# Kernel tuning notes

Measured on AMD Instinct MI355X. Metric: run time of the kernel, lower is better.

The kernel has to match this reference:

```python
import jax, jax.numpy as jnp
import numpy as np

HID = 128
IN = 4

def _lstm_cell(x, h, c, Wih, Whh, bih, bhh):
    # PyTorch LSTMCell: gates ordered i, f, g, o
    gates = x @ Wih.T + bih + h @ Whh.T + bhh  # [B, 4*HID]
    i, f, g, o = jnp.split(gates, 4, axis=-1)
    c_new = jax.nn.sigmoid(f) * c + jax.nn.sigmoid(i) * jnp.tanh(g)
    h_new = jax.nn.sigmoid(o) * jnp.tanh(c_new)
    return h_new, c_new


def setup_inputs() -> dict:
    key = jax.random.key(0)
    ks = jax.random.split(key, 12)
    T, B = 2048, 2048
    s = 1.0 / np.sqrt(HID)  # torch LSTMCell/Linear init scale (1/sqrt(hidden))
    u = lambda k, shape, sc: jax.random.uniform(k, shape, jnp.float32, -sc, sc)
    inp = {
        "input": jax.random.normal(ks[0], (T, B, IN), jnp.float32),
        "future": 0,
        "W_ih1": u(ks[1], (4 * HID, IN), s),
        "W_hh1": u(ks[2], (4 * HID, HID), s),
        "b_ih1": u(ks[3], (4 * HID,), s),
        "b_hh1": u(ks[4], (4 * HID,), s),
        "W_ih2": u(ks[5], (4 * HID, HID), s),
        "W_hh2": u(ks[6], (4 * HID, HID), s),
        "b_ih2": u(ks[7], (4 * HID,), s),
        "b_hh2": u(ks[8], (4 * HID,), s),
        "W_lin": u(ks[9], (IN, HID), s),
        "b_lin": u(ks[10], (IN,), s),
        "h0": jnp.zeros((B, HID), jnp.float32),
        "c0": jnp.zeros((B, HID), jnp.float32),
        "h02": jnp.zeros((B, HID), jnp.float32),
        "c02": jnp.zeros((B, HID), jnp.float32),
    }
    return inp


def reference(input, future, W_ih1, W_hh1, b_ih1, b_hh1, W_ih2, W_hh2, b_ih2, b_hh2,
              W_lin, b_lin, h0, c0, h02, c02):
    # alpha=1 default => teacher forcing on every step (branch never taken), future=0
    def step(carry, x_t):
        h1, c1, h2, c2 = carry
        h1, c1 = _lstm_cell(x_t, h1, c1, W_ih1, W_hh1, b_ih1, b_hh1)
        h2, c2 = _lstm_cell(h1, h2, c2, W_ih2, W_hh2, b_ih2, b_hh2)
        out = h2 @ W_lin.T + b_lin  # [B, 4]
        return (h1, c1, h2, c2), out

    _, outputs = jax.lax.scan(step, (h0, c0, h02, c02), input)
    return outputs  # [T, B, 4]
```

## Files before the change

kernel.cpp:

```cpp
#include <hip/hip_runtime.h>

#define T_STEPS 2048
#define BATCH   2048
#define HIDN    128

typedef short v8s __attribute__((ext_vector_type(8)));
typedef float v4f __attribute__((ext_vector_type(4)));
typedef unsigned short u16;
typedef unsigned int   u32;

#define LDS_W1    0
#define LDS_H1    131072
#define LDS_H2    (131072 + 8192)
#define LDS_TOTAL (131072 + 16384)

__device__ __forceinline__ u16 f2bf(float x) {
    u32 u = __float_as_uint(x);
    u32 r = (u + 0x7FFFu + ((u >> 16) & 1u)) >> 16;
    return (u16)r;
}
__device__ __forceinline__ float rcpf(float x) { return __builtin_amdgcn_rcpf(x); }
__device__ __forceinline__ float sigf(float x) { return rcpf(1.0f + __expf(-x)); }
__device__ __forceinline__ float tanhf_(float x) {
    float e = __expf(2.0f * x);
    return 1.0f - 2.0f * rcpf(e + 1.0f);
}
__device__ __forceinline__ int fragoff(int r, int k) {
    return ((k >> 5) << 10) + ((((k >> 3) & 3) * 16 + r) << 4) + ((k & 7) << 1);
}

__global__ __launch_bounds__(512, 2) void lstm_seq_kernel(
    const float* __restrict__ input,
    const float* __restrict__ W_ih1, const float* __restrict__ W_hh1,
    const float* __restrict__ b_ih1, const float* __restrict__ b_hh1,
    const float* __restrict__ W_ih2, const float* __restrict__ W_hh2,
    const float* __restrict__ b_ih2, const float* __restrict__ b_hh2,
    const float* __restrict__ W_lin, const float* __restrict__ b_lin,
    const float* __restrict__ h0,  const float* __restrict__ c0,
    const float* __restrict__ h02, const float* __restrict__ c02,
    float* __restrict__ out)
{
    extern __shared__ char smem[];
    const int tid = threadIdx.x;
    const int w   = tid >> 6;
    const int l   = tid & 63;
    const int u   = l & 15;
    const int q   = l >> 4;
    const int b0  = blockIdx.x * 8;
    const bool low = (q < 2);
    const int j   = w * 16 + u;

    for (int e = tid; e < 4096; e += 512)
        ((float*)(smem + LDS_H1))[e] = 0.0f;
    __syncthreads();
    for (int e = tid; e < 1024; e += 512) {
        int m = e >> 7, jj = e & 127;
        u16 hv1 = f2bf(h0 [(b0 + m) * HIDN + jj]);
        u16 hv2 = f2bf(h02[(b0 + m) * HIDN + jj]);
        int fo = fragoff(m, jj);
        *(u16*)(smem + LDS_H1 + 4096 + fo)       = hv1;
        *(u16*)(smem + LDS_H1 + 4096 + fo + 128) = hv1;
        *(u16*)(smem + LDS_H2 + 4096 + fo)       = hv2;
    }

    #pragma unroll
    for (int tl = 0; tl < 4; ++tl) {
        int r = tl * 128 + j;
        #pragma unroll
        for (int kt = 0; kt < 4; ++kt) {
            const float* src = W_hh1 + r * HIDN + kt * 32 + q * 8;
            v8s f;
            #pragma unroll
            for (int b = 0; b < 8; ++b) f[b] = (short)f2bf(src[b]);
            *(v8s*)(smem + LDS_W1 + (((w * 4 + tl) * 4 + kt) << 10) + l * 16) = f;
        }
    }

    v8s w2[4][8];
    #pragma unroll
    for (int tl = 0; tl < 4; ++tl) {
        int r = tl * 128 + j;
        #pragma unroll
        for (int kt = 0; kt < 8; ++kt) {
            const float* src = (kt < 4) ? (W_ih2 + r * HIDN + kt * 32 + q * 8)
                                        : (W_hh2 + r * HIDN + (kt - 4) * 32 + q * 8);
            v8s f;
            #pragma unroll
            for (int b = 0; b < 8; ++b) f[b] = (short)f2bf(src[b]);
            w2[tl][kt] = f;
        }
    }
    v8s wx[4];
    #pragma unroll
    for (int tl = 0; tl < 4; ++tl) {
        int r = tl * 128 + j;
        v8s f;
        #pragma unroll
        for (int b = 0; b < 8; ++b) {
            int k = q * 8 + b;
            f[b] = (k < 4) ? (short)f2bf(W_ih1[r * 4 + k]) : (short)0;
        }
        wx[tl] = f;
    }
    v8s wlin[4];
    if (w == 7) {
        #pragma unroll
        for (int kt = 0; kt < 4; ++kt) {
            v8s f;
            #pragma unroll
            for (int b = 0; b < 8; ++b) {
                int kk = kt * 32 + q * 8 + b;
                f[b] = (u < 4) ? (short)f2bf(W_lin[u * HIDN + kk]) : (short)0;
            }
            wlin[kt] = f;
        }
    }

    float bg[4];
    #pragma unroll
    for (int g = 0; g < 4; ++g)
        bg[g] = low ? (b_ih2[g * 128 + j] + b_hh2[g * 128 + j])
                    : (b_ih1[g * 128 + j] + b_hh1[g * 128 + j]);
    float blin = (w == 7 && u < 4) ? b_lin[u] : 0.0f;
    float c[4];
    #pragma unroll
    for (int d = 0; d < 4; ++d) {
        int m = low ? (4 * q + d) : (4 * (q - 2) + d);
        c[d] = low ? c02[(b0 + m) * HIDN + j] : c0[(b0 + m) * HIDN + j];
    }
    float4 xcur = {0, 0, 0, 0}, xnext = {0, 0, 0, 0};
    if (q == 0 && u >= 8)
        xcur = *(const float4*)(input + (long)(b0 + u - 8) * 4);

    const int cb = fragoff(0, j);
    __syncthreads();

    for (int s = 0; s <= T_STEPS; ++s) {
        const char* h1r = smem + LDS_H1 + ((s - 1) & 1) * 4096;
        const char* h2r = smem + LDS_H2 + (s & 1) * 4096;

        v8s a1[4];
        #pragma unroll
        for (int kt = 0; kt < 4; ++kt)
            a1[kt] = *(const v8s*)(h1r + (kt << 10) + l * 16);

        v4f accL2[4], accL1[4];

        if (s >= 1) {
            v8s a2[4];
            #pragma unroll
            for (int kt = 0; kt < 4; ++kt)
                a2[kt] = *(const v8s*)(h2r + (kt << 10) + l * 16);
            #pragma unroll
            for (int tl = 0; tl < 4; ++tl) {
                v4f a = {0.f, 0.f, 0.f, 0.f};
                #pragma unroll
                for (int kt = 0; kt < 4; ++kt)
                    a = __builtin_amdgcn_mfma_f32_16x16x32_bf16(a1[kt], w2[tl][kt], a, 0, 0, 0);
                #pragma unroll
                for (int kt = 0; kt < 4; ++kt)
                    a = __builtin_amdgcn_mfma_f32_16x16x32_bf16(a2[kt], w2[tl][kt + 4], a, 0, 0, 0);
                accL2[tl] = a;
            }
            if (w == 7 && s >= 2) {
                v4f oa = {0.f, 0.f, 0.f, 0.f};
                #pragma unroll
                for (int kt = 0; kt < 4; ++kt)
                    oa = __builtin_amdgcn_mfma_f32_16x16x32_bf16(a2[kt], wlin[kt], oa, 0, 0, 0);
                if (low && u < 4) {
                    #pragma unroll
                    for (int d = 0; d < 4; ++d)
                        out[((long)(s - 2) * BATCH + b0 + 4 * q + d) * 4 + u] = oa[d] + blin;
                }
            }
        }

        if (s < T_STEPS) {
            v8s ax = {0, 0, 0, 0, 0, 0, 0, 0};
            if (q == 0 && u >= 8) {
                ax[0] = (short)f2bf(xcur.x); ax[1] = (short)f2bf(xcur.y);
                ax[2] = (short)f2bf(xcur.z); ax[3] = (short)f2bf(xcur.w);
            }
            if (q == 0 && u >= 8 && s + 1 < T_STEPS)
                xnext = *(const float4*)(input + ((long)(s + 1) * BATCH + b0 + u - 8) * 4);
            #pragma unroll
            for (int tl = 0; tl < 4; ++tl) {
                v4f a = {0.f, 0.f, 0.f, 0.f};
                #pragma unroll
                for (int kt = 0; kt < 4; ++kt) {
                    v8s wf = *(const v8s*)(smem + LDS_W1 + (((w * 4 + tl) * 4 + kt) << 10) + l * 16);
                    a = __builtin_amdgcn_mfma_f32_16x16x32_bf16(a1[kt], wf, a, 0, 0, 0);
                }
                a = __builtin_amdgcn_mfma_f32_16x16x32_bf16(ax, wx[tl], a, 0, 0, 0);
                accL1[tl] = a;
            }
        }

        bool act_en = low ? (s >= 1) : (s < T_STEPS);
        if (act_en) {
            int rbase = low ? (4 * q) : (4 * (q - 2));
            char* hw = (char*)smem + (low ? (LDS_H2 + ((s - 1) & 1) * 4096)
                                          : (LDS_H1 + (s & 1) * 4096));
            #pragma unroll
            for (int d = 0; d < 4; ++d) {
                float gI = (low ? accL2[0][d] : accL1[0][d]) + bg[0];
                float gF = (low ? accL2[1][d] : accL1[1][d]) + bg[1];
                float gG = (low ? accL2[2][d] : accL1[2][d]) + bg[2];
                float gO = (low ? accL2[3][d] : accL1[3][d]) + bg[3];
                float si = sigf(gI), sf = sigf(gF), tg = tanhf_(gG), so = sigf(gO);
                c[d] = sf * c[d] + si * tg;
                float h = so * tanhf_(c[d]);
                u16 hb = f2bf(h);
                int r = rbase + d;
                *(u16*)(hw + cb + (r << 4)) = hb;
                if (!low) *(u16*)(hw + cb + (r << 4) + 128) = hb;
            }
        }
        xcur = xnext;
        __syncthreads();
    }

    if (w == 7) {
        const char* h2r = smem + LDS_H2 + ((T_STEPS - 1) & 1) * 4096;
        v4f oa = {0.f, 0.f, 0.f, 0.f};
        #pragma unroll
        for (int kt = 0; kt < 4; ++kt) {
            v8s a = *(const v8s*)(h2r + (kt << 10) + l * 16);
            oa = __builtin_amdgcn_mfma_f32_16x16x32_bf16(a, wlin[kt], oa, 0, 0, 0);
        }
        if (low && u < 4) {
            #pragma unroll
            for (int d = 0; d < 4; ++d)
                out[((long)(T_STEPS - 1) * BATCH + b0 + 4 * q + d) * 4 + u] = oa[d] + blin;
        }
    }
}

extern "C" void kernel_launch(void* const* d_in, const int* in_sizes, int n_in,
                              void* d_out, int out_size, void* d_ws, size_t ws_size,
                              hipStream_t stream) {
    const float* input = (const float*)d_in[0];
    const float* W_ih1 = (const float*)d_in[2];
    const float* W_hh1 = (const float*)d_in[3];
    const float* b_ih1 = (const float*)d_in[4];
    const float* b_hh1 = (const float*)d_in[5];
    const float* W_ih2 = (const float*)d_in[6];
    const float* W_hh2 = (const float*)d_in[7];
    const float* b_ih2 = (const float*)d_in[8];
    const float* b_hh2 = (const float*)d_in[9];
    const float* W_lin = (const float*)d_in[10];
    const float* b_lin = (const float*)d_in[11];
    const float* h0    = (const float*)d_in[12];
    const float* c0    = (const float*)d_in[13];
    const float* h02   = (const float*)d_in[14];
    const float* c02   = (const float*)d_in[15];
    float* out = (float*)d_out;

    (void)hipFuncSetAttribute((const void*)lstm_seq_kernel,
                              hipFuncAttributeMaxDynamicSharedMemorySize, LDS_TOTAL);
    lstm_seq_kernel<<<BATCH / 8, 512, LDS_TOTAL, stream>>>(
        input, W_ih1, W_hh1, b_ih1, b_hh1, W_ih2, W_hh2, b_ih2, b_hh2,
        W_lin, b_lin, h0, c0, h02, c02, out);
}
```

Before: 3.563 ms.

## Move most W_hh1 fragments into registers and interleave layer MFMAs

Three of the four k-tiles of W_hh1 now stay in registers, and only the last k-tile, the input weights and W_lin are kept in LDS. This cuts the LDS footprint and the number of LDS weight reads per step. The MFMA loop is restructured to walk k-tiles once and feed both layer-1 and layer-2 accumulators from each h1 fragment, so independent MFMA chains are interleaved. The activation code is split per layer. The cost is much higher VGPR pressure, which risks spilling or breaking the 2-blocks-per-CU launch bound.

```diff
diff --git a/kernel.cpp b/kernel.cpp
--- a/kernel.cpp
+++ b/kernel.cpp
@@ -9,10 +9,12 @@
 typedef unsigned short u16;
 typedef unsigned int   u32;
 
-#define LDS_W1    0
-#define LDS_H1    131072
-#define LDS_H2    (131072 + 8192)
-#define LDS_TOTAL (131072 + 16384)
+#define LDS_W1K3  0
+#define LDS_WX    32768
+#define LDS_WLIN  65536
+#define LDS_H1    69632
+#define LDS_H2    77824
+#define LDS_TOTAL 86016
 
 __device__ __forceinline__ u16 f2bf(float x) {
     u32 u = __float_as_uint(x);
@@ -66,13 +68,33 @@
     #pragma unroll
     for (int tl = 0; tl < 4; ++tl) {
         int r = tl * 128 + j;
+        {
+            const float* src = W_hh1 + r * HIDN + 3 * 32 + q * 8;
+            v8s f;
+            #pragma unroll
+            for (int b = 0; b < 8; ++b) f[b] = (short)f2bf(src[b]);
+            *(v8s*)(smem + LDS_W1K3 + ((w * 4 + tl) << 10) + l * 16) = f;
+        }
+        {
+            v8s f;
+            #pragma unroll
+            for (int b = 0; b < 8; ++b) {
+                int k = q * 8 + b;
+                f[b] = (k < 4) ? (short)f2bf(W_ih1[r * 4 + k]) : (short)0;
+            }
+            *(v8s*)(smem + LDS_WX + ((w * 4 + tl) << 10) + l * 16) = f;
+        }
+    }
+    if (w == 7) {
         #pragma unroll
         for (int kt = 0; kt < 4; ++kt) {
-            const float* src = W_hh1 + r * HIDN + kt * 32 + q * 8;
-            v8s f;
-            #pragma unroll
-            for (int b = 0; b < 8; ++b) f[b] = (short)f2bf(src[b]);
-            *(v8s*)(smem + LDS_W1 + (((w * 4 + tl) * 4 + kt) << 10) + l * 16) = f;
+            v8s f;
+            #pragma unroll
+            for (int b = 0; b < 8; ++b) {
+                int kk = kt * 32 + q * 8 + b;
+                f[b] = (u < 4) ? (short)f2bf(W_lin[u * HIDN + kk]) : (short)0;
+            }
+            *(v8s*)(smem + LDS_WLIN + (kt << 10) + l * 16) = f;
         }
     }
 
@@ -90,29 +112,17 @@
             w2[tl][kt] = f;
         }
     }
-    v8s wx[4];
+    v8s w1r[4][3];
     #pragma unroll
     for (int tl = 0; tl < 4; ++tl) {
         int r = tl * 128 + j;
-        v8s f;
-        #pragma unroll
-        for (int b = 0; b < 8; ++b) {
-            int k = q * 8 + b;
-            f[b] = (k < 4) ? (short)f2bf(W_ih1[r * 4 + k]) : (short)0;
-        }
-        wx[tl] = f;
-    }
-    v8s wlin[4];
-    if (w == 7) {
-        #pragma unroll
-        for (int kt = 0; kt < 4; ++kt) {
-            v8s f;
-            #pragma unroll
-            for (int b = 0; b < 8; ++b) {
-                int kk = kt * 32 + q * 8 + b;
-                f[b] = (u < 4) ? (short)f2bf(W_lin[u * HIDN + kk]) : (short)0;
-            }
-            wlin[kt] = f;
+        #pragma unroll
+        for (int kt = 0; kt < 3; ++kt) {
+            const float* src = W_hh1 + r * HIDN + kt * 32 + q * 8;
+            v8s f;
+            #pragma unroll
+            for (int b = 0; b < 8; ++b) f[b] = (short)f2bf(src[b]);
+            w1r[tl][kt] = f;
         }
     }
 
@@ -132,90 +142,109 @@
     if (q == 0 && u >= 8)
         xcur = *(const float4*)(input + (long)(b0 + u - 8) * 4);
 
-    const int cb = fragoff(0, j);
     __syncthreads();
 
     for (int s = 0; s <= T_STEPS; ++s) {
         const char* h1r = smem + LDS_H1 + ((s - 1) & 1) * 4096;
         const char* h2r = smem + LDS_H2 + (s & 1) * 4096;
-
-        v8s a1[4];
-        #pragma unroll
-        for (int kt = 0; kt < 4; ++kt)
-            a1[kt] = *(const v8s*)(h1r + (kt << 10) + l * 16);
-
-        v4f accL2[4], accL1[4];
-
-        if (s >= 1) {
-            v8s a2[4];
-            #pragma unroll
-            for (int kt = 0; kt < 4; ++kt)
-                a2[kt] = *(const v8s*)(h2r + (kt << 10) + l * 16);
-            #pragma unroll
-            for (int tl = 0; tl < 4; ++tl) {
-                v4f a = {0.f, 0.f, 0.f, 0.f};
+        const bool doL1 = (s < T_STEPS);
+        const bool doL2 = (s >= 1);
+
+        if (q == 0 && u >= 8 && s + 1 < T_STEPS)
+            xnext = *(const float4*)(input + ((long)(s + 1) * BATCH + b0 + u - 8) * 4);
+
+        v4f acc1[4] = {{0,0,0,0},{0,0,0,0},{0,0,0,0},{0,0,0,0}};
+        v4f acc2[4] = {{0,0,0,0},{0,0,0,0},{0,0,0,0},{0,0,0,0}};
+
+        #pragma unroll
+        for (int kt = 0; kt < 4; ++kt) {
+            v8s a1k = *(const v8s*)(h1r + (kt << 10) + l * 16);
+            if (doL2) {
                 #pragma unroll
-                for (int kt = 0; kt < 4; ++kt)
-                    a = __builtin_amdgcn_mfma_f32_16x16x32_bf16(a1[kt], w2[tl][kt], a, 0, 0, 0);
+                for (int tl = 0; tl < 4; ++tl)
+                    acc2[tl] = __builtin_amdgcn_mfma_f32_16x16x32_bf16(a1k, w2[tl][kt], acc2[tl], 0, 0, 0);
+            }
+            if (doL1) {
+                if (kt < 3) {
+                    #pragma unroll
+                    for (int tl = 0; tl < 4; ++tl)
+                        acc1[tl] = __builtin_amdgcn_mfma_f32_16x16x32_bf16(a1k, w1r[tl][kt], acc1[tl], 0, 0, 0);
+                } else {
+                    #pragma unroll
+                    for (int tl = 0; tl < 4; ++tl) {
+                        v8s wf = *(const v8s*)(smem + LDS_W1K3 + ((w * 4 + tl) << 10) + l * 16);
+                        acc1[tl] = __builtin_amdgcn_mfma_f32_16x16x32_bf16(a1k, wf, acc1[tl], 0, 0, 0);
+                    }
+                }
+            }
+        }
+
+        v4f oa = {0.f, 0.f, 0.f, 0.f};
+        if (doL2) {
+            #pragma unroll
+            for (int kt = 0; kt < 4; ++kt) {
+                v8s a2k = *(const v8s*)(h2r + (kt << 10) + l * 16);
                 #pragma unroll
-                for (int kt = 0; kt < 4; ++kt)
-                    a = __builtin_amdgcn_mfma_f32_16x16x32_bf16(a2[kt], w2[tl][kt + 4], a, 0, 0, 0);
-                accL2[tl] = a;
-            }
-            if (w == 7 && s >= 2) {
-                v4f oa = {0.f, 0.f, 0.f, 0.f};
+                for (int tl = 0; tl < 4; ++tl)
+                    acc2[tl] = __builtin_amdgcn_mfma_f32_16x16x32_bf16(a2k, w2[tl][kt + 4], acc2[tl], 0, 0, 0);
+                if (w == 7) {
+                    v8s wl = *(const v8s*)(smem + LDS_WLIN + (kt << 10) + l * 16);
+                    oa = __builtin_amdgcn_mfma_f32_16x16x32_bf16(a2k, wl, oa, 0, 0, 0);
+                }
+            }
+            if (w == 7 && s >= 2 && low && u < 4) {
                 #pragma unroll
-                for (int kt = 0; kt < 4; ++kt)
-                    oa = __builtin_amdgcn_mfma_f32_16x16x32_bf16(a2[kt], wlin[kt], oa, 0, 0, 0);
-                if (low && u < 4) {
-                    #pragma unroll
-                    for (int d = 0; d < 4; ++d)
-                        out[((long)(s - 2) * BATCH + b0 + 4 * q + d) * 4 + u] = oa[d] + blin;
-                }
-            }
-        }
-
-        if (s < T_STEPS) {
+                for (int d = 0; d < 4; ++d)
+                    out[((long)(s - 2) * BATCH + b0 + 4 * q + d) * 4 + u] = oa[d] + blin;
+            }
+        }
+
+        if (low && doL2) {
+            char* hw = (char*)smem + LDS_H2 + ((s - 1) & 1) * 4096;
+            #pragma unroll
+            for (int d = 0; d < 4; ++d) {
+                float gI = acc2[0][d] + bg[0];
+                float gF = acc2[1][d] + bg[1];
+                float gG = acc2[2][d] + bg[2];
+                float gO = acc2[3][d] + bg[3];
+                float si = sigf(gI), sf = sigf(gF), tg = tanhf_(gG), so = sigf(gO);
+                c[d] = sf * c[d] + si * tg;
+                u16 hb = f2bf(so * tanhf_(c[d]));
+                int r = 4 * q + d;
+                *(u16*)(hw + fragoff(r, j)) = hb;
+            }
+        }
+
+        if (doL1) {
             v8s ax = {0, 0, 0, 0, 0, 0, 0, 0};
             if (q == 0 && u >= 8) {
                 ax[0] = (short)f2bf(xcur.x); ax[1] = (short)f2bf(xcur.y);
                 ax[2] = (short)f2bf(xcur.z); ax[3] = (short)f2bf(xcur.w);
             }
-            if (q == 0 && u >= 8 && s + 1 < T_STEPS)
-                xnext = *(const float4*)(input + ((long)(s + 1) * BATCH + b0 + u - 8) * 4);
             #pragma unroll
             for (int tl = 0; tl < 4; ++tl) {
-                v4f a = {0.f, 0.f, 0.f, 0.f};
-                #pragma unroll
-                for (int kt = 0; kt < 4; ++kt) {
-                    v8s wf = *(const v8s*)(smem + LDS_W1 + (((w * 4 + tl) * 4 + kt) << 10) + l * 16);
-                    a = __builtin_amdgcn_mfma_f32_16x16x32_bf16(a1[kt], wf, a, 0, 0, 0);
-                }
-                a = __builtin_amdgcn_mfma_f32_16x16x32_bf16(ax, wx[tl], a, 0, 0, 0);
-                accL1[tl] = a;
-            }
-        }
-
-        bool act_en = low ? (s >= 1) : (s < T_STEPS);
-        if (act_en) {
-            int rbase = low ? (4 * q) : (4 * (q - 2));
-            char* hw = (char*)smem + (low ? (LDS_H2 + ((s - 1) & 1) * 4096)
-                                          : (LDS_H1 + (s & 1) * 4096));
+                v8s wxf = *(const v8s*)(smem + LDS_WX + ((w * 4 + tl) << 10) + l * 16);
+                acc1[tl] = __builtin_amdgcn_mfma_f32_16x16x32_bf16(ax, wxf, acc1[tl], 0, 0, 0);
+            }
+        }
+
+        if (!low && doL1) {
+            char* hw = (char*)smem + LDS_H1 + (s & 1) * 4096;
             #pragma unroll
             for (int d = 0; d < 4; ++d) {
-                float gI = (low ? accL2[0][d] : accL1[0][d]) + bg[0];
-                float gF = (low ? accL2[1][d] : accL1[1][d]) + bg[1];
-                float gG = (low ? accL2[2][d] : accL1[2][d]) + bg[2];
-                float gO = (low ? accL2[3][d] : accL1[3][d]) + bg[3];
+                float gI = acc1[0][d] + bg[0];
+                float gF = acc1[1][d] + bg[1];
+                float gG = acc1[2][d] + bg[2];
+                float gO = acc1[3][d] + bg[3];
                 float si = sigf(gI), sf = sigf(gF), tg = tanhf_(gG), so = sigf(gO);
                 c[d] = sf * c[d] + si * tg;
-                float h = so * tanhf_(c[d]);
-                u16 hb = f2bf(h);
-                int r = rbase + d;
-                *(u16*)(hw + cb + (r << 4)) = hb;
-                if (!low) *(u16*)(hw + cb + (r << 4) + 128) = hb;
-            }
-        }
+                u16 hb = f2bf(so * tanhf_(c[d]));
+                int r = 4 * (q - 2) + d;
+                *(u16*)(hw + fragoff(r, j))     = hb;
+                *(u16*)(hw + fragoff(r + 8, j)) = hb;
+            }
+        }
+
         xcur = xnext;
         __syncthreads();
     }
@@ -225,8 +254,9 @@
         v4f oa = {0.f, 0.f, 0.f, 0.f};
         #pragma unroll
         for (int kt = 0; kt < 4; ++kt) {
-            v8s a = *(const v8s*)(h2r + (kt << 10) + l * 16);
-            oa = __builtin_amdgcn_mfma_f32_16x16x32_bf16(a, wlin[kt], oa, 0, 0, 0);
+            v8s a2k = *(const v8s*)(h2r + (kt << 10) + l * 16);
+            v8s wl  = *(const v8s*)(smem + LDS_WLIN + (kt << 10) + l * 16);
+            oa = __builtin_amdgcn_mfma_f32_16x16x32_bf16(a2k, wl, oa, 0, 0, 0);
         }
         if (low && u < 4) {
             #pragma unroll
```

Result: slower. 6.152 ms (+72.7%).
